# Kernel optimization log

Measured on AMD Instinct MI355X. Metric: run time of the kernel, lower is better.

Reference implementation:

```python
import jax, jax.numpy as jnp
import numpy as np

N_NODES = 100000
N_EDGES = 1600000
HIDDEN = 128


def setup_inputs() -> dict:
    key = jax.random.key(0)
    k1, k2, k3 = jax.random.split(key, 3)
    pos = jax.random.normal(k1, (N_NODES, 3), dtype=jnp.float32)
    edge_index = jax.random.randint(k2, (2, N_EDGES), 0, N_NODES, dtype=jnp.int64)
    vector_features = jax.random.normal(k3, (N_NODES, 3, HIDDEN), dtype=jnp.float32)
    return {"pos": pos, "edge_index": edge_index, "vector_features": vector_features}


def reference(pos, edge_index, vector_features):
    # pos: (N,3); edge_index: (2,E); vector_features: (N,3,H) (unused by original math)
    H = vector_features.shape[-1]
    n_nodes = pos.shape[0]
    row, col = edge_index[0], edge_index[1]

    edge_vec = pos[col] - pos[row]                                  # (E,3)
    edge_dist = jnp.linalg.norm(edge_vec, axis=-1, keepdims=True) + 1e-8
    unit_vec = edge_vec / edge_dist                                 # (E,3)

    # scatter-add of unit vectors to both endpoints
    direction_units = (jnp.zeros((n_nodes, 3), dtype=pos.dtype)
                       .at[row].add(unit_vec)
                       .at[col].add(-unit_vec))                     # (N,3)

    # sum over spatial dim of du*du -> squared norm, broadcast to hidden
    angular_info = jnp.broadcast_to(
        jnp.sum(direction_units * direction_units, axis=1, keepdims=True),
        (n_nodes, H))                                               # (N,H)

    # vectorized per-edge dihedral: project v_i, v_j off the edge direction
    v_i = direction_units[row]                                      # (E,3)
    v_j = direction_units[col]                                      # (E,3)
    dot_vi = jnp.sum(v_i * unit_vec, axis=-1, keepdims=True)
    dot_vj = jnp.sum(v_j * (-unit_vec), axis=-1, keepdims=True)
    w_ij = v_i - dot_vi * unit_vec
    w_ji = v_j - dot_vj * (-unit_vec)
    dihedral_val = jnp.sum(w_ij * w_ji, axis=-1, keepdims=True)     # (E,1)
    dihedral_info = jnp.broadcast_to(dihedral_val, (edge_index.shape[1], H))

    return (angular_info, dihedral_info, direction_units)
```

## Files before the change

### kernel.cpp

```cpp
#include <hip/hip_runtime.h>
#include <math.h>

#define N_NODES 100000
#define N_EDGES 1600000
#define HIDDEN 128

#define NBINS      256
#define BIN_NODES  391
#define BIN_CAP    16384
#define A_THREADS  1024
#define A_EPT      2
#define A_EPB      (A_THREADS * A_EPT)
#define A_BLOCKS   ((N_EDGES + A_EPB - 1) / A_EPB)
#define B_THREADS  1024

typedef float vfloat4 __attribute__((ext_vector_type(4)));

__global__ void zero_cursors_kernel(unsigned* __restrict__ cur) {
    cur[threadIdx.x] = 0u;
}

__global__ __launch_bounds__(A_THREADS) void bin_edges_kernel(
    const int* __restrict__ eidx,
    unsigned* __restrict__ cursors,
    unsigned* __restrict__ region)
{
    __shared__ unsigned cnt[NBINS];
    __shared__ unsigned base[NBINS];
    if (threadIdx.x < NBINS) cnt[threadIdx.x] = 0u;
    __syncthreads();

    const int e0 = blockIdx.x * A_EPB + threadIdx.x;

    bool     val[A_EPT];
    unsigned br[A_EPT], orow[A_EPT], bc[A_EPT], ocol[A_EPT];

    #pragma unroll
    for (int k = 0; k < A_EPT; ++k) {
        int e = e0 + k * A_THREADS;
        val[k] = (e < N_EDGES);
        if (val[k]) {
            unsigned r = (unsigned)eidx[e];
            unsigned c = (unsigned)eidx[N_EDGES + e];
            br[k] = r / BIN_NODES;
            bc[k] = c / BIN_NODES;
            orow[k] = atomicAdd(&cnt[br[k]], 1u);
            ocol[k] = atomicAdd(&cnt[bc[k]], 1u);
        }
    }
    __syncthreads();

    if (threadIdx.x < NBINS)
        base[threadIdx.x] = atomicAdd(&cursors[threadIdx.x], cnt[threadIdx.x]);
    __syncthreads();

    #pragma unroll
    for (int k = 0; k < A_EPT; ++k) {
        if (val[k]) {
            unsigned e = (unsigned)(e0 + k * A_THREADS);
            region[br[k] * BIN_CAP + base[br[k]] + orow[k]] = (e << 1);
            region[bc[k] * BIN_CAP + base[bc[k]] + ocol[k]] = (e << 1) | 1u;
        }
    }
}

__global__ __launch_bounds__(B_THREADS) void accumulate_kernel(
    const float* __restrict__ pos,
    const int* __restrict__ eidx,
    const unsigned* __restrict__ cursors,
    const unsigned* __restrict__ region,
    float* __restrict__ du,
    float* __restrict__ ang)
{
    __shared__ float acc[BIN_NODES * 3];
    const unsigned b = blockIdx.x;
    const unsigned nodebase = b * BIN_NODES;

    for (int i = threadIdx.x; i < BIN_NODES * 3; i += B_THREADS) acc[i] = 0.0f;
    __syncthreads();

    const unsigned n = cursors[b];
    const unsigned* __restrict__ reg = region + (size_t)b * BIN_CAP;

    for (unsigned i = threadIdx.x; i < n; i += B_THREADS) {
        unsigned rec  = reg[i];
        unsigned e    = rec >> 1;
        unsigned side = rec & 1u;
        unsigned r = (unsigned)eidx[e];
        unsigned c = (unsigned)eidx[N_EDGES + e];

        float dx = pos[c * 3 + 0] - pos[r * 3 + 0];
        float dy = pos[c * 3 + 1] - pos[r * 3 + 1];
        float dz = pos[c * 3 + 2] - pos[r * 3 + 2];
        float inv = 1.0f / (sqrtf(dx * dx + dy * dy + dz * dz) + 1e-8f);
        float ux = dx * inv, uy = dy * inv, uz = dz * inv;

        unsigned node = side ? c : r;
        float s = side ? -1.0f : 1.0f;
        unsigned l = node - nodebase;
        atomicAdd(&acc[l * 3 + 0], s * ux);
        atomicAdd(&acc[l * 3 + 1], s * uy);
        atomicAdd(&acc[l * 3 + 2], s * uz);
    }
    __syncthreads();

    const unsigned nloc = min((unsigned)BIN_NODES,
                              (unsigned)(N_NODES - nodebase));

    for (unsigned i = threadIdx.x; i < nloc * 3; i += B_THREADS)
        du[(size_t)nodebase * 3 + i] = acc[i];

    for (unsigned j = threadIdx.x; j < nloc * 32; j += B_THREADS) {
        unsigned node = j >> 5, c4 = j & 31;
        float x = acc[node * 3 + 0];
        float y = acc[node * 3 + 1];
        float z = acc[node * 3 + 2];
        float a = x * x + y * y + z * z;
        vfloat4 v4 = {a, a, a, a};
        __builtin_nontemporal_store(v4,
            reinterpret_cast<vfloat4*>(ang + (size_t)(nodebase + node) * HIDDEN) + c4);
    }
}

__global__ void dihedral_kernel(const float* __restrict__ pos,
                                const int* __restrict__ eidx,
                                const float* __restrict__ du,
                                float* __restrict__ dih) {
    __shared__ float vals[256];
    const int e0 = blockIdx.x * 256;
    const int e  = e0 + threadIdx.x;

    {
        int r = eidx[e];
        int c = eidx[N_EDGES + e];

        float dx = pos[c * 3 + 0] - pos[r * 3 + 0];
        float dy = pos[c * 3 + 1] - pos[r * 3 + 1];
        float dz = pos[c * 3 + 2] - pos[r * 3 + 2];
        float dist = sqrtf(dx * dx + dy * dy + dz * dz) + 1e-8f;
        float inv = 1.0f / dist;
        float ux = dx * inv, uy = dy * inv, uz = dz * inv;

        float vix = du[r * 3 + 0], viy = du[r * 3 + 1], viz = du[r * 3 + 2];
        float vjx = du[c * 3 + 0], vjy = du[c * 3 + 1], vjz = du[c * 3 + 2];

        float dvi = vix * ux + viy * uy + viz * uz;
        float dvj = -(vjx * ux + vjy * uy + vjz * uz);

        float wix = vix - dvi * ux;
        float wiy = viy - dvi * uy;
        float wiz = viz - dvi * uz;
        float wjx = vjx + dvj * ux;
        float wjy = vjy + dvj * uy;
        float wjz = vjz + dvj * uz;

        vals[threadIdx.x] = wix * wjx + wiy * wjy + wiz * wjz;
    }
    __syncthreads();

    vfloat4* out = reinterpret_cast<vfloat4*>(dih + (size_t)e0 * HIDDEN);
    #pragma unroll
    for (int it = 0; it < 32; ++it) {
        int i = it * 256 + threadIdx.x;
        float v = vals[i >> 5];
        vfloat4 v4 = {v, v, v, v};
        __builtin_nontemporal_store(v4, out + i);
    }
}

__global__ void zero_du_kernel(float* __restrict__ du, int n) {
    int i = blockIdx.x * blockDim.x + threadIdx.x;
    if (i < n) du[i] = 0.0f;
}

__global__ void edge_scatter_kernel(const float* __restrict__ pos,
                                    const int* __restrict__ eidx,
                                    float* __restrict__ du) {
    int e = blockIdx.x * blockDim.x + threadIdx.x;
    if (e >= N_EDGES) return;
    int r = eidx[e];
    int c = eidx[N_EDGES + e];
    float dx = pos[c * 3 + 0] - pos[r * 3 + 0];
    float dy = pos[c * 3 + 1] - pos[r * 3 + 1];
    float dz = pos[c * 3 + 2] - pos[r * 3 + 2];
    float inv = 1.0f / (sqrtf(dx * dx + dy * dy + dz * dz) + 1e-8f);
    float ux = dx * inv, uy = dy * inv, uz = dz * inv;
    atomicAdd(&du[r * 3 + 0],  ux);
    atomicAdd(&du[r * 3 + 1],  uy);
    atomicAdd(&du[r * 3 + 2],  uz);
    atomicAdd(&du[c * 3 + 0], -ux);
    atomicAdd(&du[c * 3 + 1], -uy);
    atomicAdd(&du[c * 3 + 2], -uz);
}

__global__ void angular_kernel(const float* __restrict__ du,
                               float* __restrict__ ang) {
    int gid = blockIdx.x * blockDim.x + threadIdx.x;
    int node = gid >> 5;
    int c4   = gid & 31;
    float x = du[node * 3 + 0];
    float y = du[node * 3 + 1];
    float z = du[node * 3 + 2];
    float a = x * x + y * y + z * z;
    vfloat4 v4 = {a, a, a, a};
    __builtin_nontemporal_store(v4,
        reinterpret_cast<vfloat4*>(ang + (size_t)node * HIDDEN) + c4);
}

extern "C" void kernel_launch(void* const* d_in, const int* in_sizes, int n_in,
                              void* d_out, int out_size, void* d_ws, size_t ws_size,
                              hipStream_t stream) {
    const float* pos  = (const float*)d_in[0];
    const int*   eidx = (const int*)d_in[1];

    float* out = (float*)d_out;
    float* ang = out;
    float* dih = out + (size_t)N_NODES * HIDDEN;
    float* du  = dih + (size_t)N_EDGES * HIDDEN;

    const size_t need = 1024 + (size_t)NBINS * BIN_CAP * sizeof(unsigned);

    if (ws_size >= need) {
        unsigned* cursors = (unsigned*)d_ws;
        unsigned* region  = (unsigned*)d_ws + 256;

        zero_cursors_kernel<<<1, NBINS, 0, stream>>>(cursors);
        bin_edges_kernel<<<A_BLOCKS, A_THREADS, 0, stream>>>(eidx, cursors, region);
        accumulate_kernel<<<NBINS, B_THREADS, 0, stream>>>(pos, eidx, cursors,
                                                           region, du, ang);
    } else {
        zero_du_kernel<<<(N_NODES * 3 + 255) / 256, 256, 0, stream>>>(du, N_NODES * 3);
        edge_scatter_kernel<<<(N_EDGES + 255) / 256, 256, 0, stream>>>(pos, eidx, du);
        angular_kernel<<<(N_NODES * 32) / 256, 256, 0, stream>>>(du, ang);
    }

    dihedral_kernel<<<N_EDGES / 256, 256, 0, stream>>>(pos, eidx, du, dih);
}
```

Before: 263.2 us.

## Encode local/other node in bin records and stage bin positions in LDS

```diff
diff --git a/kernel.cpp b/kernel.cpp
--- a/kernel.cpp
+++ b/kernel.cpp
@@ -14,6 +14,7 @@
 #define A_BLOCKS   ((N_EDGES + A_EPB - 1) / A_EPB)
 #define B_THREADS  1024
 
+
 typedef float vfloat4 __attribute__((ext_vector_type(4)));
 
 __global__ void zero_cursors_kernel(unsigned* __restrict__ cur) {
@@ -30,20 +31,20 @@
     if (threadIdx.x < NBINS) cnt[threadIdx.x] = 0u;
     __syncthreads();
 
-    const int e0 = blockIdx.x * A_EPB + threadIdx.x;
-
-    bool     val[A_EPT];
-    unsigned br[A_EPT], orow[A_EPT], bc[A_EPT], ocol[A_EPT];
-
-    #pragma unroll
-    for (int k = 0; k < A_EPT; ++k) {
-        int e = e0 + k * A_THREADS;
-        val[k] = (e < N_EDGES);
-        if (val[k]) {
-            unsigned r = (unsigned)eidx[e];
-            unsigned c = (unsigned)eidx[N_EDGES + e];
-            br[k] = r / BIN_NODES;
-            bc[k] = c / BIN_NODES;
+    const int e0 = blockIdx.x * A_EPB + threadIdx.x * 2;
+    const bool valid = (e0 < N_EDGES);
+
+    unsigned r[A_EPT], c[A_EPT], br[A_EPT], bc[A_EPT], orow[A_EPT], ocol[A_EPT];
+
+    if (valid) {
+        int2 rr = *reinterpret_cast<const int2*>(eidx + e0);
+        int2 cc = *reinterpret_cast<const int2*>(eidx + N_EDGES + e0);
+        r[0] = (unsigned)rr.x; r[1] = (unsigned)rr.y;
+        c[0] = (unsigned)cc.x; c[1] = (unsigned)cc.y;
+        #pragma unroll
+        for (int k = 0; k < A_EPT; ++k) {
+            br[k] = r[k] / BIN_NODES;
+            bc[k] = c[k] / BIN_NODES;
             orow[k] = atomicAdd(&cnt[br[k]], 1u);
             ocol[k] = atomicAdd(&cnt[bc[k]], 1u);
         }
@@ -54,58 +55,68 @@
         base[threadIdx.x] = atomicAdd(&cursors[threadIdx.x], cnt[threadIdx.x]);
     __syncthreads();
 
-    #pragma unroll
-    for (int k = 0; k < A_EPT; ++k) {
-        if (val[k]) {
-            unsigned e = (unsigned)(e0 + k * A_THREADS);
-            region[br[k] * BIN_CAP + base[br[k]] + orow[k]] = (e << 1);
-            region[bc[k] * BIN_CAP + base[bc[k]] + ocol[k]] = (e << 1) | 1u;
+    if (valid) {
+        #pragma unroll
+        for (int k = 0; k < A_EPT; ++k) {
+            region[br[k] * BIN_CAP + base[br[k]] + orow[k]] =
+                ((r[k] - br[k] * BIN_NODES) << 17) | c[k];
+            region[bc[k] * BIN_CAP + base[bc[k]] + ocol[k]] =
+                ((c[k] - bc[k] * BIN_NODES) << 17) | r[k];
         }
     }
+}
+
+__device__ __forceinline__ void proc_rec(unsigned rec,
+                                         const float* __restrict__ posLDS,
+                                         const float* __restrict__ pos,
+                                         float* __restrict__ acc) {
+    unsigned other = rec & 0x1FFFFu;
+    unsigned local = rec >> 17;
+    float sx = posLDS[local * 3 + 0];
+    float sy = posLDS[local * 3 + 1];
+    float sz = posLDS[local * 3 + 2];
+    float dx = pos[other * 3 + 0] - sx;
+    float dy = pos[other * 3 + 1] - sy;
+    float dz = pos[other * 3 + 2] - sz;
+    float inv = 1.0f / (sqrtf(dx * dx + dy * dy + dz * dz) + 1e-8f);
+    atomicAdd(&acc[local * 3 + 0], dx * inv);
+    atomicAdd(&acc[local * 3 + 1], dy * inv);
+    atomicAdd(&acc[local * 3 + 2], dz * inv);
 }
 
 __global__ __launch_bounds__(B_THREADS) void accumulate_kernel(
     const float* __restrict__ pos,
-    const int* __restrict__ eidx,
     const unsigned* __restrict__ cursors,
     const unsigned* __restrict__ region,
     float* __restrict__ du,
     float* __restrict__ ang)
 {
     __shared__ float acc[BIN_NODES * 3];
+    __shared__ float posLDS[BIN_NODES * 3];
     const unsigned b = blockIdx.x;
     const unsigned nodebase = b * BIN_NODES;
+    const unsigned nloc = min((unsigned)BIN_NODES,
+                              (unsigned)(N_NODES - nodebase));
 
     for (int i = threadIdx.x; i < BIN_NODES * 3; i += B_THREADS) acc[i] = 0.0f;
+    for (unsigned i = threadIdx.x; i < nloc * 3; i += B_THREADS)
+        posLDS[i] = pos[(size_t)nodebase * 3 + i];
     __syncthreads();
 
     const unsigned n = cursors[b];
     const unsigned* __restrict__ reg = region + (size_t)b * BIN_CAP;
-
-    for (unsigned i = threadIdx.x; i < n; i += B_THREADS) {
-        unsigned rec  = reg[i];
-        unsigned e    = rec >> 1;
-        unsigned side = rec & 1u;
-        unsigned r = (unsigned)eidx[e];
-        unsigned c = (unsigned)eidx[N_EDGES + e];
-
-        float dx = pos[c * 3 + 0] - pos[r * 3 + 0];
-        float dy = pos[c * 3 + 1] - pos[r * 3 + 1];
-        float dz = pos[c * 3 + 2] - pos[r * 3 + 2];
-        float inv = 1.0f / (sqrtf(dx * dx + dy * dy + dz * dz) + 1e-8f);
-        float ux = dx * inv, uy = dy * inv, uz = dz * inv;
-
-        unsigned node = side ? c : r;
-        float s = side ? -1.0f : 1.0f;
-        unsigned l = node - nodebase;
-        atomicAdd(&acc[l * 3 + 0], s * ux);
-        atomicAdd(&acc[l * 3 + 1], s * uy);
-        atomicAdd(&acc[l * 3 + 2], s * uz);
-    }
-    __syncthreads();
-
-    const unsigned nloc = min((unsigned)BIN_NODES,
-                              (unsigned)(N_NODES - nodebase));
+    const unsigned n4 = n & ~3u;
+
+    for (unsigned i = threadIdx.x * 4; i < n4; i += B_THREADS * 4) {
+        uint4 rc = *reinterpret_cast<const uint4*>(reg + i);
+        proc_rec(rc.x, posLDS, pos, acc);
+        proc_rec(rc.y, posLDS, pos, acc);
+        proc_rec(rc.z, posLDS, pos, acc);
+        proc_rec(rc.w, posLDS, pos, acc);
+    }
+    for (unsigned i = n4 + threadIdx.x; i < n; i += B_THREADS)
+        proc_rec(reg[i], posLDS, pos, acc);
+    __syncthreads();
 
     for (unsigned i = threadIdx.x; i < nloc * 3; i += B_THREADS)
         du[(size_t)nodebase * 3 + i] = acc[i];
@@ -226,7 +237,7 @@
 
         zero_cursors_kernel<<<1, NBINS, 0, stream>>>(cursors);
         bin_edges_kernel<<<A_BLOCKS, A_THREADS, 0, stream>>>(eidx, cursors, region);
-        accumulate_kernel<<<NBINS, B_THREADS, 0, stream>>>(pos, eidx, cursors,
+        accumulate_kernel<<<NBINS, B_THREADS, 0, stream>>>(pos, cursors,
                                                            region, du, ang);
     } else {
         zero_du_kernel<<<(N_NODES * 3 + 255) / 256, 256, 0, stream>>>(du, N_NODES * 3);
```

Result: faster. 256.6 us (-2.5%).
